# Kernel tuning notes

Measured on AMD Instinct MI355X. Metric: run time of the kernel, lower is better.

The kernel has to match this reference:

```python
import jax, jax.numpy as jnp
import numpy as np

D_MODEL = 1024
N_HEADS = 16
HEAD_DIM = D_MODEL // N_HEADS


def setup_inputs() -> dict:
    key = jax.random.key(0)
    ks = jax.random.split(key, 6)
    B, S = 2, 2048
    scale = 1.0 / np.sqrt(D_MODEL)
    x = jax.random.normal(ks[0], (B, S, D_MODEL), dtype=jnp.float32)
    Wq = jax.random.normal(ks[1], (D_MODEL, D_MODEL), dtype=jnp.float32) * scale
    Wk = jax.random.normal(ks[2], (D_MODEL, D_MODEL), dtype=jnp.float32) * scale
    Wv = jax.random.normal(ks[3], (D_MODEL, D_MODEL), dtype=jnp.float32) * scale
    Wo = jax.random.normal(ks[4], (D_MODEL, D_MODEL), dtype=jnp.float32) * scale
    bo = jax.random.normal(ks[5], (D_MODEL,), dtype=jnp.float32) * 0.02
    return {"x": x, "Wq": Wq, "Wk": Wk, "Wv": Wv, "Wo": Wo, "bo": bo}


def reference(x, Wq, Wk, Wv, Wo, bo):
    B, S, _ = x.shape
    H, hd = N_HEADS, HEAD_DIM
    # qkv projections (no bias, qkv_bias=False)
    q = (x @ Wq).reshape(B, S, H, hd).transpose(0, 2, 1, 3)  # [B,H,S,hd]
    k = (x @ Wk).reshape(B, S, H, hd).transpose(0, 2, 1, 3)
    v = (x @ Wv).reshape(B, S, H, hd).transpose(0, 2, 1, 3)
    scores = jnp.einsum('bhqd,bhkd->bhqk', q, k)  # [B,H,S,S]
    causal = jnp.tril(jnp.ones((S, S), dtype=bool))  # True = keep
    scores = jnp.where(causal, scores, -jnp.inf)
    weights = jax.nn.softmax(scores / np.sqrt(hd), axis=-1)
    # dropout p=0.0 -> identity
    ctx = jnp.einsum('bhqk,bhkd->bhqd', weights, v)  # [B,H,S,hd]
    ctx = ctx.transpose(0, 2, 1, 3).reshape(B, S, H * hd)
    return ctx @ Wo + bo
```

## Files before the change

kernel.cpp:

```cpp
#include <hip/hip_runtime.h>
#include <hip/hip_bf16.h>
#include <stdint.h>

#define SEQ    2048
#define BATCH  2
#define DMODEL 1024
#define NHEADS 16
#define HDIM   64
#define MROWS  (BATCH*SEQ)

typedef __attribute__((ext_vector_type(8))) short bf16x8;
typedef __attribute__((ext_vector_type(4))) short bf16x4;
typedef __attribute__((ext_vector_type(4))) float f32x4;

__device__ inline void global_to_lds16(const void* g, void* l) {
  __builtin_amdgcn_global_load_lds(
      (const __attribute__((address_space(1))) uint32_t*)g,
      (__attribute__((address_space(3))) uint32_t*)l, 16, 0, 0);
}

__device__ inline unsigned short f2bf_bits(float f) {
  __hip_bfloat16 h = __float2bfloat16(f);
  return *(unsigned short*)&h;
}

__global__ void cvt_x(const float* __restrict__ x, __hip_bfloat16* __restrict__ xb) {
  int i = (blockIdx.x * 256 + threadIdx.x) * 4;
  float4 v = *(const float4*)(x + i);
  ushort4 o;
  o.x = f2bf_bits(v.x); o.y = f2bf_bits(v.y);
  o.z = f2bf_bits(v.z); o.w = f2bf_bits(v.w);
  *(ushort4*)(xb + i) = o;
}

__global__ void trans_w(const float* __restrict__ Wq, const float* __restrict__ Wk,
                        const float* __restrict__ Wv, const float* __restrict__ Wo,
                        __hip_bfloat16* __restrict__ Wqkv_t, __hip_bfloat16* __restrict__ Wo_t) {
  __shared__ float tile[32][33];
  int z = blockIdx.z;
  const float* W = (z == 0) ? Wq : (z == 1) ? Wk : (z == 2) ? Wv : Wo;
  __hip_bfloat16* dst = (z < 3) ? (Wqkv_t + (size_t)z * 1024 * 1024) : Wo_t;
  int k0 = blockIdx.x * 32, n0 = blockIdx.y * 32;
  int tx = threadIdx.x & 31, ty = threadIdx.x >> 5;
#pragma unroll
  for (int r = 0; r < 4; r++)
    tile[ty + r * 8][tx] = W[(size_t)(k0 + ty + r * 8) * 1024 + n0 + tx];
  __syncthreads();
#pragma unroll
  for (int r = 0; r < 4; r++)
    dst[(size_t)(n0 + ty + r * 8) * 1024 + k0 + tx] = __float2bfloat16(tile[tx][ty + r * 8]);
}

template <int TN, bool OUT_BF16, int MINW, bool FUSE_VT>
__global__ __launch_bounds__(256, MINW)
void gemm_kernel(const __hip_bfloat16* __restrict__ A, const __hip_bfloat16* __restrict__ Bt,
                 void* __restrict__ C, const float* __restrict__ bias, int ldc,
                 __hip_bfloat16* __restrict__ Vt) {
  __shared__ __hip_bfloat16 Asl[128 * 64];
  __shared__ __hip_bfloat16 Bsl[TN * 64];

  const int t = threadIdx.x;
  const int lane = t & 63;
  const int w = t >> 6;
  constexpr int MI = (TN == 128) ? 4 : 2;
  const int wrow = (TN == 128) ? (w >> 1) * 64 : w * 32;
  const int wcol = (TN == 128) ? (w & 1) * 64 : 0;
  const int m0 = blockIdx.y * 128;
  const int n0 = blockIdx.x * TN;

  f32x4 acc[MI][4];
#pragma unroll
  for (int i = 0; i < MI; i++)
#pragma unroll
    for (int j = 0; j < 4; j++) acc[i][j] = (f32x4){0.f, 0.f, 0.f, 0.f};

  const int srow = lane >> 3;
  const int sjc = (lane & 7) ^ srow;
  const int fm = lane & 15;
  const int g4 = lane >> 4;

  for (int k0 = 0; k0 < 1024; k0 += 64) {
#pragma unroll
    for (int i = 0; i < 4; i++) {
      int seg = i * 4 + w;
      int r = seg * 8 + srow;
      global_to_lds16(A + (size_t)(m0 + r) * 1024 + k0 + sjc * 8,
                      (void*)(Asl + seg * 512 + lane * 8));
    }
#pragma unroll
    for (int i = 0; i < TN / 32; i++) {
      int seg = i * 4 + w;
      int r = seg * 8 + srow;
      global_to_lds16(Bt + (size_t)(n0 + r) * 1024 + k0 + sjc * 8,
                      (void*)(Bsl + seg * 512 + lane * 8));
    }
    __syncthreads();
#pragma unroll
    for (int kb = 0; kb < 2; kb++) {
      bf16x8 af[MI], bfr[4];
#pragma unroll
      for (int mi = 0; mi < MI; mi++) {
        int row = wrow + mi * 16 + fm;
        af[mi] = *(const bf16x8*)(Asl + row * 64 + (((kb * 4 + g4) ^ (row & 7)) << 3));
      }
#pragma unroll
      for (int ni = 0; ni < 4; ni++) {
        int row = wcol + ni * 16 + fm;
        bfr[ni] = *(const bf16x8*)(Bsl + row * 64 + (((kb * 4 + g4) ^ (row & 7)) << 3));
      }
#pragma unroll
      for (int mi = 0; mi < MI; mi++)
#pragma unroll
        for (int ni = 0; ni < 4; ni++)
          acc[mi][ni] = __builtin_amdgcn_mfma_f32_16x16x32_bf16(af[mi], bfr[ni], acc[mi][ni], 0, 0, 0);
    }
    __syncthreads();
  }

  const bool vt_block = FUSE_VT && (n0 >= 2048);
#pragma unroll
  for (int mi = 0; mi < MI; mi++) {
    int mb = m0 + wrow + mi * 16 + g4 * 4;
#pragma unroll
    for (int ni = 0; ni < 4; ni++) {
      int n = n0 + wcol + ni * 16 + fm;
      if (vt_block) {
        int nv = n - 2048;
        int bhh = (mb >> 11) * 16 + (nv >> 6);
        int d = nv & 63;
        int s = mb & 2047;
        unsigned short u[4];
#pragma unroll
        for (int r = 0; r < 4; r++) u[r] = f2bf_bits(acc[mi][ni][r]);
        *(ushort4*)(Vt + ((size_t)bhh * 64 + d) * 2048 + s) = *(const ushort4*)u;
      } else {
        float bv = OUT_BF16 ? 0.f : bias[n];
#pragma unroll
        for (int r = 0; r < 4; r++) {
          if (OUT_BF16)
            ((__hip_bfloat16*)C)[(size_t)(mb + r) * ldc + n] = __float2bfloat16(acc[mi][ni][r]);
          else
            ((float*)C)[(size_t)(mb + r) * ldc + n] = acc[mi][ni][r] + bv;
        }
      }
    }
  }
}

__global__ __launch_bounds__(256, 2)
void attn_kernel(const __hip_bfloat16* __restrict__ QKV,
                 const __hip_bfloat16* __restrict__ Vt,
                 __hip_bfloat16* __restrict__ ctx) {
  __shared__ __hip_bfloat16 Klds[2][128 * 64];
  __shared__ __hip_bfloat16 Vlds[2][64 * 128];

  const int t = threadIdx.x;
  const int lane = t & 63;
  const int w = t >> 6;
  const int L = blockIdx.x;
  const int bh = (L & 7) + 8 * ((L >> 3) & 3);
  const int jraw = L >> 5;
  const int jb = (jraw < 8) ? jraw : 23 - jraw;
  const int qtab[2] = { jb, 31 - jb };
  const int b = bh >> 4, h = bh & 15;
  const int fm = lane & 15;
  const int g4 = lane >> 4;
  const int fk = g4 * 8;
  const size_t rowb = (size_t)b * SEQ;
  const float c = 0.18033688011112042f;

  const int krr = lane >> 3;
  const int kjc = (lane & 7) ^ krr;
  const int vrr = lane >> 4;

  bf16x8 qf[2][2];
#pragma unroll
  for (int hh = 0; hh < 2; hh++) {
    const __hip_bfloat16* qp = QKV + (rowb + qtab[hh] * 64 + w * 16 + fm) * 3072 + h * 64 + fk;
    bf16x8 r0 = *(const bf16x8*)qp;
    bf16x8 r1 = *(const bf16x8*)(qp + 32);
#pragma unroll
    for (int i = 0; i < 8; i++) {
      float f0 = __uint_as_float(((unsigned)(unsigned short)r0[i]) << 16) * c;
      float f1 = __uint_as_float(((unsigned)(unsigned short)r1[i]) << 16) * c;
      r0[i] = (short)f2bf_bits(f0);
      r1[i] = (short)f2bf_bits(f1);
    }
    qf[hh][0] = r0; qf[hh][1] = r1;
  }

  bf16x4 ones4;
#pragma unroll
  for (int i = 0; i < 4; i++) ones4[i] = (short)0x3F80;

  f32x4 acc[2][4];
  f32x4 lacc[2];
#pragma unroll
  for (int hh = 0; hh < 2; hh++) {
    lacc[hh] = (f32x4){0.f, 0.f, 0.f, 0.f};
#pragma unroll
    for (int d = 0; d < 4; d++) acc[hh][d] = (f32x4){0.f, 0.f, 0.f, 0.f};
  }

  auto stage = [&](int pt, int bufi) {
    const int kt0 = pt * 128;
#pragma unroll
    for (int i = 0; i < 4; i++) {
      int seg = i * 4 + w;
      int kr = seg * 8 + krr;
      global_to_lds16(QKV + (rowb + kt0 + kr) * 3072 + 1024 + h * 64 + kjc * 8,
                      (void*)(&Klds[bufi][0] + seg * 512 + lane * 8));
      int vd = seg * 4 + vrr;
      int vjc = (lane & 15) ^ ((seg & 1) * 4 + vrr);
      global_to_lds16(Vt + ((size_t)bh * 64 + vd) * 2048 + kt0 + vjc * 8,
                      (void*)(&Vlds[bufi][0] + seg * 512 + lane * 8));
    }
  };

  const int lastt = qtab[1];
  const int lastp = lastt >> 1;
  stage(0, 0);
  for (int pt = 0; pt <= lastp; ++pt) {
    __syncthreads();
    if (pt < lastp) stage(pt + 1, (pt + 1) & 1);
    const __hip_bfloat16* Kb = &Klds[pt & 1][0];
    const __hip_bfloat16* Vb = &Vlds[pt & 1][0];

#pragma unroll
    for (int sc = 0; sc < 2; sc++) {
      const int kts = pt * 2 + sc;
      if (kts > lastt) break;
      const bool act0 = (kts <= qtab[0]);

      f32x4 st1[4], st0[4];
#pragma unroll
      for (int ns = 0; ns < 4; ns++) {
        st1[ns] = (f32x4){0.f, 0.f, 0.f, 0.f};
        st0[ns] = (f32x4){0.f, 0.f, 0.f, 0.f};
      }
#pragma unroll
      for (int kk = 0; kk < 2; kk++) {
        bf16x8 kf[4];
#pragma unroll
        for (int ns = 0; ns < 4; ns++) {
          int row = sc * 64 + ns * 16 + fm;
          kf[ns] = *(const bf16x8*)(Kb + row * 64 + (((kk * 4 + g4) ^ (fm & 7)) << 3));
        }
#pragma unroll
        for (int ns = 0; ns < 4; ns++)
          st1[ns] = __builtin_amdgcn_mfma_f32_16x16x32_bf16(kf[ns], qf[1][kk], st1[ns], 0, 0, 0);
        if (act0)
#pragma unroll
          for (int ns = 0; ns < 4; ns++)
            st0[ns] = __builtin_amdgcn_mfma_f32_16x16x32_bf16(kf[ns], qf[0][kk], st0[ns], 0, 0, 0);
      }

      bf16x4 vf[4][4];
#pragma unroll
      for (int dd = 0; dd < 4; dd++)
#pragma unroll
        for (int ns = 0; ns < 4; ns++) {
          int ch = sc * 8 + ns * 2 + (g4 >> 1);
          vf[dd][ns] = *(const bf16x4*)(Vb + (dd * 16 + fm) * 128 +
                                        ((ch ^ (fm & 7)) << 3) + (g4 & 1) * 4);
        }

      auto half = [&](const f32x4 (&st)[4], int hh) {
        const bool diag = (kts == qtab[hh]);
#pragma unroll
        for (int ns = 0; ns < 4; ns++) {
          float e[4];
#pragma unroll
          for (int r = 0; r < 4; r++) {
            float p = __builtin_amdgcn_exp2f(st[ns][r]);
            if (diag) {
              int ktl = ns * 16 + g4 * 4 + r;
              p = (ktl > w * 16 + fm) ? 0.f : p;
            }
            e[r] = p;
          }
          unsigned lo = __builtin_amdgcn_perm(__builtin_bit_cast(unsigned, e[1]),
                                              __builtin_bit_cast(unsigned, e[0]), 0x07060302u);
          unsigned hi = __builtin_amdgcn_perm(__builtin_bit_cast(unsigned, e[3]),
                                              __builtin_bit_cast(unsigned, e[2]), 0x07060302u);
          uint2 pp; pp.x = lo; pp.y = hi;
          bf16x4 pf = __builtin_bit_cast(bf16x4, pp);
          lacc[hh] = __builtin_amdgcn_mfma_f32_16x16x16bf16_1k(pf, ones4, lacc[hh], 0, 0, 0);
#pragma unroll
          for (int dd = 0; dd < 4; dd++)
            acc[hh][dd] = __builtin_amdgcn_mfma_f32_16x16x16bf16_1k(pf, vf[dd][ns], acc[hh][dd], 0, 0, 0);
        }
      };
      half(st1, 1);
      if (act0) half(st0, 0);
    }
  }

#pragma unroll
  for (int hh = 0; hh < 2; hh++) {
    float rl[4];
#pragma unroll
    for (int r = 0; r < 4; r++) rl[r] = __builtin_amdgcn_rcpf(lacc[hh][r]);
#pragma unroll
    for (int dd = 0; dd < 4; dd++)
#pragma unroll
      for (int r = 0; r < 4; r++) {
        int q = qtab[hh] * 64 + w * 16 + g4 * 4 + r;
        ctx[(rowb + q) * 1024 + h * 64 + dd * 16 + fm] =
            __float2bfloat16(acc[hh][dd][r] * rl[r]);
      }
  }
}

extern "C" void kernel_launch(void* const* d_in, const int* in_sizes, int n_in,
                              void* d_out, int out_size, void* d_ws, size_t ws_size,
                              hipStream_t stream) {
  const float* x  = (const float*)d_in[0];
  const float* Wq = (const float*)d_in[1];
  const float* Wk = (const float*)d_in[2];
  const float* Wv = (const float*)d_in[3];
  const float* Wo = (const float*)d_in[4];
  const float* bo = (const float*)d_in[5];
  float* out = (float*)d_out;

  char* ws = (char*)d_ws;
  __hip_bfloat16* xb     = (__hip_bfloat16*)(ws);
  __hip_bfloat16* Wqkv_t = (__hip_bfloat16*)(ws + (8ull  << 20));
  __hip_bfloat16* Wo_t   = (__hip_bfloat16*)(ws + (14ull << 20));
  __hip_bfloat16* QKV    = (__hip_bfloat16*)(ws + (16ull << 20));
  __hip_bfloat16* ctxb   = (__hip_bfloat16*)(ws + (40ull << 20));
  __hip_bfloat16* Vt     = (__hip_bfloat16*)(ws + (48ull << 20));

  cvt_x<<<dim3(MROWS * DMODEL / (256 * 4)), dim3(256), 0, stream>>>(x, xb);
  trans_w<<<dim3(32, 32, 4), dim3(256), 0, stream>>>(Wq, Wk, Wv, Wo, Wqkv_t, Wo_t);
  gemm_kernel<128, true, 3, true><<<dim3(24, 32), dim3(256), 0, stream>>>(
      xb, Wqkv_t, (void*)QKV, nullptr, 3072, Vt);
  attn_kernel<<<dim3(512), dim3(256), 0, stream>>>(QKV, Vt, ctxb);
  gemm_kernel<64, false, 2, false><<<dim3(16, 32), dim3(256), 0, stream>>>(
      ctxb, Wo_t, (void*)out, bo, 1024, nullptr);
}
```

Baseline: 167.3 us.

## Split attention into one query tile per block and merge prep kernels

The attention kernel no longer pairs two query tiles (jb and 31-jb) per block. Each block now handles a single 64-row query tile, with smaller 64-key K/V stages, a launch of 1024 blocks, and a launch bound of 3 blocks per CU. Blocks are ordered so the longest causal tiles come first. Separately, the x-conversion and weight-transpose kernels are merged into one launch to drop one kernel launch. The split gives more, lighter blocks and higher occupancy, at the cost of losing the balanced pairing, reloading K/V per query tile, and doing more barriers per unit of work.

```diff
diff --git a/kernel.cpp b/kernel.cpp
--- a/kernel.cpp
+++ b/kernel.cpp
@@ -24,23 +24,26 @@
   return *(unsigned short*)&h;
 }
 
-__global__ void cvt_x(const float* __restrict__ x, __hip_bfloat16* __restrict__ xb) {
-  int i = (blockIdx.x * 256 + threadIdx.x) * 4;
-  float4 v = *(const float4*)(x + i);
-  ushort4 o;
-  o.x = f2bf_bits(v.x); o.y = f2bf_bits(v.y);
-  o.z = f2bf_bits(v.z); o.w = f2bf_bits(v.w);
-  *(ushort4*)(xb + i) = o;
-}
-
-__global__ void trans_w(const float* __restrict__ Wq, const float* __restrict__ Wk,
-                        const float* __restrict__ Wv, const float* __restrict__ Wo,
-                        __hip_bfloat16* __restrict__ Wqkv_t, __hip_bfloat16* __restrict__ Wo_t) {
+__global__ void prep_kernel(const float* __restrict__ x, __hip_bfloat16* __restrict__ xb,
+                            const float* __restrict__ Wq, const float* __restrict__ Wk,
+                            const float* __restrict__ Wv, const float* __restrict__ Wo,
+                            __hip_bfloat16* __restrict__ Wqkv_t, __hip_bfloat16* __restrict__ Wo_t) {
   __shared__ float tile[32][33];
-  int z = blockIdx.z;
+  if (blockIdx.x < 4096) {
+    int i = (blockIdx.x * 256 + threadIdx.x) * 4;
+    float4 v = *(const float4*)(x + i);
+    ushort4 o;
+    o.x = f2bf_bits(v.x); o.y = f2bf_bits(v.y);
+    o.z = f2bf_bits(v.z); o.w = f2bf_bits(v.w);
+    *(ushort4*)(xb + i) = o;
+    return;
+  }
+  int idx = blockIdx.x - 4096;
+  int z = idx >> 10;
+  int rem = idx & 1023;
   const float* W = (z == 0) ? Wq : (z == 1) ? Wk : (z == 2) ? Wv : Wo;
   __hip_bfloat16* dst = (z < 3) ? (Wqkv_t + (size_t)z * 1024 * 1024) : Wo_t;
-  int k0 = blockIdx.x * 32, n0 = blockIdx.y * 32;
+  int k0 = (rem & 31) * 32, n0 = (rem >> 5) * 32;
   int tx = threadIdx.x & 31, ty = threadIdx.x >> 5;
 #pragma unroll
   for (int r = 0; r < 4; r++)
@@ -147,21 +150,19 @@
   }
 }
 
-__global__ __launch_bounds__(256, 2)
+__global__ __launch_bounds__(256, 3)
 void attn_kernel(const __hip_bfloat16* __restrict__ QKV,
                  const __hip_bfloat16* __restrict__ Vt,
                  __hip_bfloat16* __restrict__ ctx) {
-  __shared__ __hip_bfloat16 Klds[2][128 * 64];
-  __shared__ __hip_bfloat16 Vlds[2][64 * 128];
+  __shared__ __hip_bfloat16 Klds[2][64 * 64];
+  __shared__ __hip_bfloat16 Vlds[2][64 * 64];
 
   const int t = threadIdx.x;
   const int lane = t & 63;
   const int w = t >> 6;
   const int L = blockIdx.x;
   const int bh = (L & 7) + 8 * ((L >> 3) & 3);
-  const int jraw = L >> 5;
-  const int jb = (jraw < 8) ? jraw : 23 - jraw;
-  const int qtab[2] = { jb, 31 - jb };
+  const int qt = 31 - (L >> 5);
   const int b = bh >> 4, h = bh & 15;
   const int fm = lane & 15;
   const int g4 = lane >> 4;
@@ -171,12 +172,10 @@
 
   const int krr = lane >> 3;
   const int kjc = (lane & 7) ^ krr;
-  const int vrr = lane >> 4;
-
-  bf16x8 qf[2][2];
-#pragma unroll
-  for (int hh = 0; hh < 2; hh++) {
-    const __hip_bfloat16* qp = QKV + (rowb + qtab[hh] * 64 + w * 16 + fm) * 3072 + h * 64 + fk;
+
+  bf16x8 qf[2];
+  {
+    const __hip_bfloat16* qp = QKV + (rowb + qt * 64 + w * 16 + fm) * 3072 + h * 64 + fk;
     bf16x8 r0 = *(const bf16x8*)qp;
     bf16x8 r1 = *(const bf16x8*)(qp + 32);
 #pragma unroll
@@ -186,130 +185,95 @@
       r0[i] = (short)f2bf_bits(f0);
       r1[i] = (short)f2bf_bits(f1);
     }
-    qf[hh][0] = r0; qf[hh][1] = r1;
+    qf[0] = r0; qf[1] = r1;
   }
 
   bf16x4 ones4;
 #pragma unroll
   for (int i = 0; i < 4; i++) ones4[i] = (short)0x3F80;
 
-  f32x4 acc[2][4];
-  f32x4 lacc[2];
-#pragma unroll
-  for (int hh = 0; hh < 2; hh++) {
-    lacc[hh] = (f32x4){0.f, 0.f, 0.f, 0.f};
-#pragma unroll
-    for (int d = 0; d < 4; d++) acc[hh][d] = (f32x4){0.f, 0.f, 0.f, 0.f};
-  }
-
-  auto stage = [&](int pt, int bufi) {
-    const int kt0 = pt * 128;
-#pragma unroll
-    for (int i = 0; i < 4; i++) {
-      int seg = i * 4 + w;
-      int kr = seg * 8 + krr;
-      global_to_lds16(QKV + (rowb + kt0 + kr) * 3072 + 1024 + h * 64 + kjc * 8,
+  f32x4 acc[4];
+  f32x4 lacc = (f32x4){0.f, 0.f, 0.f, 0.f};
+#pragma unroll
+  for (int d = 0; d < 4; d++) acc[d] = (f32x4){0.f, 0.f, 0.f, 0.f};
+
+  auto stage = [&](int kts, int bufi) {
+    const int kt0 = kts * 64;
+#pragma unroll
+    for (int i = 0; i < 2; i++) {
+      int seg = w + i * 4;
+      int r = seg * 8 + krr;
+      global_to_lds16(QKV + (rowb + kt0 + r) * 3072 + 1024 + h * 64 + kjc * 8,
                       (void*)(&Klds[bufi][0] + seg * 512 + lane * 8));
-      int vd = seg * 4 + vrr;
-      int vjc = (lane & 15) ^ ((seg & 1) * 4 + vrr);
-      global_to_lds16(Vt + ((size_t)bh * 64 + vd) * 2048 + kt0 + vjc * 8,
+      global_to_lds16(Vt + ((size_t)bh * 64 + r) * 2048 + kt0 + kjc * 8,
                       (void*)(&Vlds[bufi][0] + seg * 512 + lane * 8));
     }
   };
 
-  const int lastt = qtab[1];
-  const int lastp = lastt >> 1;
   stage(0, 0);
-  for (int pt = 0; pt <= lastp; ++pt) {
+  for (int kts = 0; kts <= qt; ++kts) {
     __syncthreads();
-    if (pt < lastp) stage(pt + 1, (pt + 1) & 1);
-    const __hip_bfloat16* Kb = &Klds[pt & 1][0];
-    const __hip_bfloat16* Vb = &Vlds[pt & 1][0];
-
-#pragma unroll
-    for (int sc = 0; sc < 2; sc++) {
-      const int kts = pt * 2 + sc;
-      if (kts > lastt) break;
-      const bool act0 = (kts <= qtab[0]);
-
-      f32x4 st1[4], st0[4];
+    if (kts < qt) stage(kts + 1, (kts + 1) & 1);
+    const __hip_bfloat16* Kb = &Klds[kts & 1][0];
+    const __hip_bfloat16* Vb = &Vlds[kts & 1][0];
+
+    f32x4 st[4];
+#pragma unroll
+    for (int ns = 0; ns < 4; ns++) st[ns] = (f32x4){0.f, 0.f, 0.f, 0.f};
+#pragma unroll
+    for (int kk = 0; kk < 2; kk++) {
 #pragma unroll
       for (int ns = 0; ns < 4; ns++) {
-        st1[ns] = (f32x4){0.f, 0.f, 0.f, 0.f};
-        st0[ns] = (f32x4){0.f, 0.f, 0.f, 0.f};
-      }
-#pragma unroll
-      for (int kk = 0; kk < 2; kk++) {
-        bf16x8 kf[4];
-#pragma unroll
-        for (int ns = 0; ns < 4; ns++) {
-          int row = sc * 64 + ns * 16 + fm;
-          kf[ns] = *(const bf16x8*)(Kb + row * 64 + (((kk * 4 + g4) ^ (fm & 7)) << 3));
+        bf16x8 kf = *(const bf16x8*)(Kb + (ns * 16 + fm) * 64 + (((kk * 4 + g4) ^ (fm & 7)) << 3));
+        st[ns] = __builtin_amdgcn_mfma_f32_16x16x32_bf16(kf, qf[kk], st[ns], 0, 0, 0);
+      }
+    }
+
+    bf16x4 vf[4][4];
+#pragma unroll
+    for (int dd = 0; dd < 4; dd++)
+#pragma unroll
+      for (int ns = 0; ns < 4; ns++)
+        vf[dd][ns] = *(const bf16x4*)(Vb + (dd * 16 + fm) * 64 +
+                                      (((2 * ns + (g4 >> 1)) ^ (fm & 7)) << 3) + (g4 & 1) * 4);
+
+    const bool diag = (kts == qt);
+#pragma unroll
+    for (int ns = 0; ns < 4; ns++) {
+      float e[4];
+#pragma unroll
+      for (int r = 0; r < 4; r++) {
+        float p = __builtin_amdgcn_exp2f(st[ns][r]);
+        if (diag) {
+          int ktl = ns * 16 + g4 * 4 + r;
+          p = (ktl > w * 16 + fm) ? 0.f : p;
         }
-#pragma unroll
-        for (int ns = 0; ns < 4; ns++)
-          st1[ns] = __builtin_amdgcn_mfma_f32_16x16x32_bf16(kf[ns], qf[1][kk], st1[ns], 0, 0, 0);
-        if (act0)
-#pragma unroll
-          for (int ns = 0; ns < 4; ns++)
-            st0[ns] = __builtin_amdgcn_mfma_f32_16x16x32_bf16(kf[ns], qf[0][kk], st0[ns], 0, 0, 0);
-      }
-
-      bf16x4 vf[4][4];
+        e[r] = p;
+      }
+      unsigned lo = __builtin_amdgcn_perm(__builtin_bit_cast(unsigned, e[1]),
+                                          __builtin_bit_cast(unsigned, e[0]), 0x07060302u);
+      unsigned hi = __builtin_amdgcn_perm(__builtin_bit_cast(unsigned, e[3]),
+                                          __builtin_bit_cast(unsigned, e[2]), 0x07060302u);
+      uint2 pp; pp.x = lo; pp.y = hi;
+      bf16x4 pf = __builtin_bit_cast(bf16x4, pp);
+      lacc = __builtin_amdgcn_mfma_f32_16x16x16bf16_1k(pf, ones4, lacc, 0, 0, 0);
 #pragma unroll
       for (int dd = 0; dd < 4; dd++)
-#pragma unroll
-        for (int ns = 0; ns < 4; ns++) {
-          int ch = sc * 8 + ns * 2 + (g4 >> 1);
-          vf[dd][ns] = *(const bf16x4*)(Vb + (dd * 16 + fm) * 128 +
-                                        ((ch ^ (fm & 7)) << 3) + (g4 & 1) * 4);
-        }
-
-      auto half = [&](const f32x4 (&st)[4], int hh) {
-        const bool diag = (kts == qtab[hh]);
-#pragma unroll
-        for (int ns = 0; ns < 4; ns++) {
-          float e[4];
-#pragma unroll
-          for (int r = 0; r < 4; r++) {
-            float p = __builtin_amdgcn_exp2f(st[ns][r]);
-            if (diag) {
-              int ktl = ns * 16 + g4 * 4 + r;
-              p = (ktl > w * 16 + fm) ? 0.f : p;
-            }
-            e[r] = p;
-          }
-          unsigned lo = __builtin_amdgcn_perm(__builtin_bit_cast(unsigned, e[1]),
-                                              __builtin_bit_cast(unsigned, e[0]), 0x07060302u);
-          unsigned hi = __builtin_amdgcn_perm(__builtin_bit_cast(unsigned, e[3]),
-                                              __builtin_bit_cast(unsigned, e[2]), 0x07060302u);
-          uint2 pp; pp.x = lo; pp.y = hi;
-          bf16x4 pf = __builtin_bit_cast(bf16x4, pp);
-          lacc[hh] = __builtin_amdgcn_mfma_f32_16x16x16bf16_1k(pf, ones4, lacc[hh], 0, 0, 0);
-#pragma unroll
-          for (int dd = 0; dd < 4; dd++)
-            acc[hh][dd] = __builtin_amdgcn_mfma_f32_16x16x16bf16_1k(pf, vf[dd][ns], acc[hh][dd], 0, 0, 0);
-        }
-      };
-      half(st1, 1);
-      if (act0) half(st0, 0);
-    }
-  }
-
-#pragma unroll
-  for (int hh = 0; hh < 2; hh++) {
-    float rl[4];
-#pragma unroll
-    for (int r = 0; r < 4; r++) rl[r] = __builtin_amdgcn_rcpf(lacc[hh][r]);
-#pragma unroll
-    for (int dd = 0; dd < 4; dd++)
-#pragma unroll
-      for (int r = 0; r < 4; r++) {
-        int q = qtab[hh] * 64 + w * 16 + g4 * 4 + r;
-        ctx[(rowb + q) * 1024 + h * 64 + dd * 16 + fm] =
-            __float2bfloat16(acc[hh][dd][r] * rl[r]);
-      }
-  }
+        acc[dd] = __builtin_amdgcn_mfma_f32_16x16x16bf16_1k(pf, vf[dd][ns], acc[dd], 0, 0, 0);
+    }
+  }
+
+  float rl[4];
+#pragma unroll
+  for (int r = 0; r < 4; r++) rl[r] = __builtin_amdgcn_rcpf(lacc[r]);
+#pragma unroll
+  for (int dd = 0; dd < 4; dd++)
+#pragma unroll
+    for (int r = 0; r < 4; r++) {
+      int q = qt * 64 + w * 16 + g4 * 4 + r;
+      ctx[(rowb + q) * 1024 + h * 64 + dd * 16 + fm] =
+          __float2bfloat16(acc[dd][r] * rl[r]);
+    }
 }
 
 extern "C" void kernel_launch(void* const* d_in, const int* in_sizes, int n_in,
@@ -331,11 +295,10 @@
   __hip_bfloat16* ctxb   = (__hip_bfloat16*)(ws + (40ull << 20));
   __hip_bfloat16* Vt     = (__hip_bfloat16*)(ws + (48ull << 20));
 
-  cvt_x<<<dim3(MROWS * DMODEL / (256 * 4)), dim3(256), 0, stream>>>(x, xb);
-  trans_w<<<dim3(32, 32, 4), dim3(256), 0, stream>>>(Wq, Wk, Wv, Wo, Wqkv_t, Wo_t);
+  prep_kernel<<<dim3(8192), dim3(256), 0, stream>>>(x, xb, Wq, Wk, Wv, Wo, Wqkv_t, Wo_t);
   gemm_kernel<128, true, 3, true><<<dim3(24, 32), dim3(256), 0, stream>>>(
       xb, Wqkv_t, (void*)QKV, nullptr, 3072, Vt);
-  attn_kernel<<<dim3(512), dim3(256), 0, stream>>>(QKV, Vt, ctxb);
+  attn_kernel<<<dim3(1024), dim3(256), 0, stream>>>(QKV, Vt, ctxb);
   gemm_kernel<64, false, 2, false><<<dim3(16, 32), dim3(256), 0, stream>>>(
       ctxb, Wo_t, (void*)out, bo, 1024, nullptr);
 }
```

New measurement: 169.0 us. About the same (+1.0%).

## Merge prep kernels and shrink attention KV tiles to 64 with earlier fragment loads

Applied to the files above, without the earlier changes.

Merges the x conversion and weight transpose into one launch to save one kernel launch. Rewrites the attention loop to stage 64-key K/V tiles instead of 128. It reads all K and V fragments into registers before issuing the next tile's async load, so the prefetch overlaps with the MFMA work. This halves LDS use per block, which may raise occupancy, but needs twice as many barriers and more registers for the fragments held across iterations.

```diff
diff --git a/kernel.cpp b/kernel.cpp
--- a/kernel.cpp
+++ b/kernel.cpp
@@ -24,23 +24,26 @@
   return *(unsigned short*)&h;
 }
 
-__global__ void cvt_x(const float* __restrict__ x, __hip_bfloat16* __restrict__ xb) {
-  int i = (blockIdx.x * 256 + threadIdx.x) * 4;
-  float4 v = *(const float4*)(x + i);
-  ushort4 o;
-  o.x = f2bf_bits(v.x); o.y = f2bf_bits(v.y);
-  o.z = f2bf_bits(v.z); o.w = f2bf_bits(v.w);
-  *(ushort4*)(xb + i) = o;
-}
-
-__global__ void trans_w(const float* __restrict__ Wq, const float* __restrict__ Wk,
-                        const float* __restrict__ Wv, const float* __restrict__ Wo,
-                        __hip_bfloat16* __restrict__ Wqkv_t, __hip_bfloat16* __restrict__ Wo_t) {
+__global__ void prep_kernel(const float* __restrict__ x, __hip_bfloat16* __restrict__ xb,
+                            const float* __restrict__ Wq, const float* __restrict__ Wk,
+                            const float* __restrict__ Wv, const float* __restrict__ Wo,
+                            __hip_bfloat16* __restrict__ Wqkv_t, __hip_bfloat16* __restrict__ Wo_t) {
   __shared__ float tile[32][33];
-  int z = blockIdx.z;
+  if (blockIdx.x < 4096) {
+    int i = (blockIdx.x * 256 + threadIdx.x) * 4;
+    float4 v = *(const float4*)(x + i);
+    ushort4 o;
+    o.x = f2bf_bits(v.x); o.y = f2bf_bits(v.y);
+    o.z = f2bf_bits(v.z); o.w = f2bf_bits(v.w);
+    *(ushort4*)(xb + i) = o;
+    return;
+  }
+  int idx = blockIdx.x - 4096;
+  int z = idx >> 10;
+  int rem = idx & 1023;
   const float* W = (z == 0) ? Wq : (z == 1) ? Wk : (z == 2) ? Wv : Wo;
   __hip_bfloat16* dst = (z < 3) ? (Wqkv_t + (size_t)z * 1024 * 1024) : Wo_t;
-  int k0 = blockIdx.x * 32, n0 = blockIdx.y * 32;
+  int k0 = (rem & 31) * 32, n0 = (rem >> 5) * 32;
   int tx = threadIdx.x & 31, ty = threadIdx.x >> 5;
 #pragma unroll
   for (int r = 0; r < 4; r++)
@@ -151,8 +154,8 @@
 void attn_kernel(const __hip_bfloat16* __restrict__ QKV,
                  const __hip_bfloat16* __restrict__ Vt,
                  __hip_bfloat16* __restrict__ ctx) {
-  __shared__ __hip_bfloat16 Klds[2][128 * 64];
-  __shared__ __hip_bfloat16 Vlds[2][64 * 128];
+  __shared__ __hip_bfloat16 Klds[2][64 * 64];
+  __shared__ __hip_bfloat16 Vlds[2][64 * 64];
 
   const int t = threadIdx.x;
   const int lane = t & 63;
@@ -171,7 +174,6 @@
 
   const int krr = lane >> 3;
   const int kjc = (lane & 7) ^ krr;
-  const int vrr = lane >> 4;
 
   bf16x8 qf[2][2];
 #pragma unroll
@@ -202,98 +204,88 @@
     for (int d = 0; d < 4; d++) acc[hh][d] = (f32x4){0.f, 0.f, 0.f, 0.f};
   }
 
-  auto stage = [&](int pt, int bufi) {
-    const int kt0 = pt * 128;
-#pragma unroll
-    for (int i = 0; i < 4; i++) {
-      int seg = i * 4 + w;
-      int kr = seg * 8 + krr;
-      global_to_lds16(QKV + (rowb + kt0 + kr) * 3072 + 1024 + h * 64 + kjc * 8,
+  auto stage = [&](int kts, int bufi) {
+    const int kt0 = kts * 64;
+#pragma unroll
+    for (int i = 0; i < 2; i++) {
+      int seg = w + i * 4;
+      int r = seg * 8 + krr;
+      global_to_lds16(QKV + (rowb + kt0 + r) * 3072 + 1024 + h * 64 + kjc * 8,
                       (void*)(&Klds[bufi][0] + seg * 512 + lane * 8));
-      int vd = seg * 4 + vrr;
-      int vjc = (lane & 15) ^ ((seg & 1) * 4 + vrr);
-      global_to_lds16(Vt + ((size_t)bh * 64 + vd) * 2048 + kt0 + vjc * 8,
+      global_to_lds16(Vt + ((size_t)bh * 64 + r) * 2048 + kt0 + kjc * 8,
                       (void*)(&Vlds[bufi][0] + seg * 512 + lane * 8));
     }
   };
 
   const int lastt = qtab[1];
-  const int lastp = lastt >> 1;
   stage(0, 0);
-  for (int pt = 0; pt <= lastp; ++pt) {
+  for (int kts = 0; kts <= lastt; ++kts) {
     __syncthreads();
-    if (pt < lastp) stage(pt + 1, (pt + 1) & 1);
-    const __hip_bfloat16* Kb = &Klds[pt & 1][0];
-    const __hip_bfloat16* Vb = &Vlds[pt & 1][0];
-
-#pragma unroll
-    for (int sc = 0; sc < 2; sc++) {
-      const int kts = pt * 2 + sc;
-      if (kts > lastt) break;
-      const bool act0 = (kts <= qtab[0]);
-
-      f32x4 st1[4], st0[4];
+    const __hip_bfloat16* Kb = &Klds[kts & 1][0];
+    const __hip_bfloat16* Vb = &Vlds[kts & 1][0];
+    const bool act0 = (kts <= qtab[0]);
+
+    bf16x8 kf[2][4];
+#pragma unroll
+    for (int kk = 0; kk < 2; kk++)
+#pragma unroll
+      for (int ns = 0; ns < 4; ns++)
+        kf[kk][ns] = *(const bf16x8*)(Kb + (ns * 16 + fm) * 64 + (((kk * 4 + g4) ^ (fm & 7)) << 3));
+    bf16x4 vf[4][4];
+#pragma unroll
+    for (int dd = 0; dd < 4; dd++)
+#pragma unroll
+      for (int ns = 0; ns < 4; ns++)
+        vf[dd][ns] = *(const bf16x4*)(Vb + (dd * 16 + fm) * 64 +
+                                      (((2 * ns + (g4 >> 1)) ^ (fm & 7)) << 3) + (g4 & 1) * 4);
+
+    if (kts < lastt) stage(kts + 1, (kts + 1) & 1);
+
+    f32x4 st1[4], st0[4];
+#pragma unroll
+    for (int ns = 0; ns < 4; ns++) {
+      st1[ns] = (f32x4){0.f, 0.f, 0.f, 0.f};
+      st0[ns] = (f32x4){0.f, 0.f, 0.f, 0.f};
+    }
+#pragma unroll
+    for (int kk = 0; kk < 2; kk++) {
+#pragma unroll
+      for (int ns = 0; ns < 4; ns++)
+        st1[ns] = __builtin_amdgcn_mfma_f32_16x16x32_bf16(kf[kk][ns], qf[1][kk], st1[ns], 0, 0, 0);
+      if (act0)
+#pragma unroll
+        for (int ns = 0; ns < 4; ns++)
+          st0[ns] = __builtin_amdgcn_mfma_f32_16x16x32_bf16(kf[kk][ns], qf[0][kk], st0[ns], 0, 0, 0);
+    }
+
+    auto half = [&](const f32x4 (&st)[4], int hh) {
+      const bool diag = (kts == qtab[hh]);
 #pragma unroll
       for (int ns = 0; ns < 4; ns++) {
-        st1[ns] = (f32x4){0.f, 0.f, 0.f, 0.f};
-        st0[ns] = (f32x4){0.f, 0.f, 0.f, 0.f};
-      }
-#pragma unroll
-      for (int kk = 0; kk < 2; kk++) {
-        bf16x8 kf[4];
-#pragma unroll
-        for (int ns = 0; ns < 4; ns++) {
-          int row = sc * 64 + ns * 16 + fm;
-          kf[ns] = *(const bf16x8*)(Kb + row * 64 + (((kk * 4 + g4) ^ (fm & 7)) << 3));
+        float e[4];
+#pragma unroll
+        for (int r = 0; r < 4; r++) {
+          float p = __builtin_amdgcn_exp2f(st[ns][r]);
+          if (diag) {
+            int ktl = ns * 16 + g4 * 4 + r;
+            p = (ktl > w * 16 + fm) ? 0.f : p;
+          }
+          e[r] = p;
         }
-#pragma unroll
-        for (int ns = 0; ns < 4; ns++)
-          st1[ns] = __builtin_amdgcn_mfma_f32_16x16x32_bf16(kf[ns], qf[1][kk], st1[ns], 0, 0, 0);
-        if (act0)
-#pragma unroll
-          for (int ns = 0; ns < 4; ns++)
-            st0[ns] = __builtin_amdgcn_mfma_f32_16x16x32_bf16(kf[ns], qf[0][kk], st0[ns], 0, 0, 0);
-      }
-
-      bf16x4 vf[4][4];
-#pragma unroll
-      for (int dd = 0; dd < 4; dd++)
-#pragma unroll
-        for (int ns = 0; ns < 4; ns++) {
-          int ch = sc * 8 + ns * 2 + (g4 >> 1);
-          vf[dd][ns] = *(const bf16x4*)(Vb + (dd * 16 + fm) * 128 +
-                                        ((ch ^ (fm & 7)) << 3) + (g4 & 1) * 4);
-        }
-
-      auto half = [&](const f32x4 (&st)[4], int hh) {
-        const bool diag = (kts == qtab[hh]);
-#pragma unroll
-        for (int ns = 0; ns < 4; ns++) {
-          float e[4];
-#pragma unroll
-          for (int r = 0; r < 4; r++) {
-            float p = __builtin_amdgcn_exp2f(st[ns][r]);
-            if (diag) {
-              int ktl = ns * 16 + g4 * 4 + r;
-              p = (ktl > w * 16 + fm) ? 0.f : p;
-            }
-            e[r] = p;
-          }
-          unsigned lo = __builtin_amdgcn_perm(__builtin_bit_cast(unsigned, e[1]),
-                                              __builtin_bit_cast(unsigned, e[0]), 0x07060302u);
-          unsigned hi = __builtin_amdgcn_perm(__builtin_bit_cast(unsigned, e[3]),
-                                              __builtin_bit_cast(unsigned, e[2]), 0x07060302u);
-          uint2 pp; pp.x = lo; pp.y = hi;
-          bf16x4 pf = __builtin_bit_cast(bf16x4, pp);
-          lacc[hh] = __builtin_amdgcn_mfma_f32_16x16x16bf16_1k(pf, ones4, lacc[hh], 0, 0, 0);
-#pragma unroll
-          for (int dd = 0; dd < 4; dd++)
-            acc[hh][dd] = __builtin_amdgcn_mfma_f32_16x16x16bf16_1k(pf, vf[dd][ns], acc[hh][dd], 0, 0, 0);
-        }
-      };
-      half(st1, 1);
-      if (act0) half(st0, 0);
-    }
+        unsigned lo = __builtin_amdgcn_perm(__builtin_bit_cast(unsigned, e[1]),
+                                            __builtin_bit_cast(unsigned, e[0]), 0x07060302u);
+        unsigned hi = __builtin_amdgcn_perm(__builtin_bit_cast(unsigned, e[3]),
+                                            __builtin_bit_cast(unsigned, e[2]), 0x07060302u);
+        uint2 pp; pp.x = lo; pp.y = hi;
+        bf16x4 pf = __builtin_bit_cast(bf16x4, pp);
+        lacc[hh] = __builtin_amdgcn_mfma_f32_16x16x16bf16_1k(pf, ones4, lacc[hh], 0, 0, 0);
+#pragma unroll
+        for (int dd = 0; dd < 4; dd++)
+          acc[hh][dd] = __builtin_amdgcn_mfma_f32_16x16x16bf16_1k(pf, vf[dd][ns], acc[hh][dd], 0, 0, 0);
+      }
+    };
+    half(st1, 1);
+    if (act0) half(st0, 0);
   }
 
 #pragma unroll
@@ -331,8 +323,7 @@
   __hip_bfloat16* ctxb   = (__hip_bfloat16*)(ws + (40ull << 20));
   __hip_bfloat16* Vt     = (__hip_bfloat16*)(ws + (48ull << 20));
 
-  cvt_x<<<dim3(MROWS * DMODEL / (256 * 4)), dim3(256), 0, stream>>>(x, xb);
-  trans_w<<<dim3(32, 32, 4), dim3(256), 0, stream>>>(Wq, Wk, Wv, Wo, Wqkv_t, Wo_t);
+  prep_kernel<<<dim3(8192), dim3(256), 0, stream>>>(x, xb, Wq, Wk, Wv, Wo, Wqkv_t, Wo_t);
   gemm_kernel<128, true, 3, true><<<dim3(24, 32), dim3(256), 0, stream>>>(
       xb, Wqkv_t, (void*)QKV, nullptr, 3072, Vt);
   attn_kernel<<<dim3(512), dim3(256), 0, stream>>>(QKV, Vt, ctxb);
```

New measurement: 163.0 us. 1.03x faster.
